# Performance work log

Measured on AMD Instinct MI355X. Metric: run time of the kernel, lower is better.

Reference implementation:

```python
import jax, jax.numpy as jnp
import numpy as np

N_ENT = 200000  # entities per graph (sr and tg)
E = 4_000_000   # triples per graph
R_SR, R_TG, D = 1000, 1200, 128


def _cosine_sim_nbyn(a, b):
    a = a * jax.lax.rsqrt(jnp.sum(a * a, -1, keepdims=True) + 1e-8)
    b = b * jax.lax.rsqrt(jnp.sum(b * b, -1, keepdims=True) + 1e-8)
    return a @ b.T


def _relation_weighting(a, b):
    # pad to square, cosine similarity, max-pool rows/cols (MuGNN RelationWeighting)
    ra, rb = a.shape[0], b.shape[0]
    n = max(ra, rb)
    a_p = jnp.pad(a, ((0, n - ra), (0, 0)))
    b_p = jnp.pad(b, ((0, n - rb), (0, 0)))
    sim = _cosine_sim_nbyn(a_p, b_p)  # [n, n]
    return jnp.max(sim, axis=1)[:ra], jnp.max(sim, axis=0)[:rb]


def _normalize_adj(rows, cols, vals, n):
    # symmetric normalization D^-1/2 A D^-1/2 on COO values
    deg = jax.ops.segment_sum(vals, rows, num_segments=n)
    d_is = jnp.where(deg > 0, jax.lax.rsqrt(jnp.maximum(deg, 1e-12)), 0.0)
    return vals * d_is[rows] * d_is[cols]


def _adjacency_side(head, tail, conf, imp, pca, n):
    # g_func_template: elementwise product of the three aligned sparse matrices
    vals = conf * imp * pca
    # + unit (identity) matrix, then normalize; coords = [edges ; diagonal]
    diag = jnp.arange(n)
    rows = jnp.concatenate([head, diag])
    cols = jnp.concatenate([tail, diag])
    allv = jnp.concatenate([vals, jnp.ones((n,), vals.dtype)])
    return _normalize_adj(rows, cols, allv, n)  # [E+n] COO values


def setup_inputs() -> dict:
    key = jax.random.key(0)
    ks = jax.random.split(key, 14)
    return {
        "rel_emb_sr": jax.random.normal(ks[0], (R_SR, D), jnp.float32),
        "rel_emb_tg": jax.random.normal(ks[1], (R_TG, D), jnp.float32),
        "conf_sr": jax.random.uniform(ks[2], (E,), jnp.float32),
        "imp_sr": jax.random.uniform(ks[3], (E,), jnp.float32),
        "pca_sr": jax.random.uniform(ks[4], (E,), jnp.float32),
        "conf_tg": jax.random.uniform(ks[5], (E,), jnp.float32),
        "imp_tg": jax.random.uniform(ks[6], (E,), jnp.float32),
        "pca_tg": jax.random.uniform(ks[7], (E,), jnp.float32),
        "head_sr": jax.random.randint(ks[8], (E,), 0, N_ENT),
        "tail_sr": jax.random.randint(ks[9], (E,), 0, N_ENT),
        "relation_sr": jax.random.randint(ks[10], (E,), 0, R_SR),
        "head_tg": jax.random.randint(ks[11], (E,), 0, N_ENT),
        "tail_tg": jax.random.randint(ks[12], (E,), 0, N_ENT),
        "relation_tg": jax.random.randint(ks[13], (E,), 0, R_TG),
    }


def reference(rel_emb_sr, rel_emb_tg, conf_sr, imp_sr, pca_sr,
              conf_tg, imp_tg, pca_tg,
              head_sr, tail_sr, relation_sr, head_tg, tail_tg, relation_tg):
    # relation weighting (computed in the original forward; g_func_template
    # discards the gathered relation attention, so relation_sr/tg do not
    # affect the adjacency values)
    rw_sr, rw_tg = _relation_weighting(rel_emb_sr, rel_emb_tg)
    adj_sr = _adjacency_side(head_sr, tail_sr, conf_sr, imp_sr, pca_sr, N_ENT)
    adj_tg = _adjacency_side(head_tg, tail_tg, conf_tg, imp_tg, pca_tg, N_ENT)
    # adjacency returned as normalized COO values on constant coords
    return adj_sr, adj_tg, rw_sr, rw_tg
```

## Files before the change

### kernel.cpp

```cpp
#include <hip/hip_runtime.h>
#include <stdint.h>

#define N_ENT 200000
#define NEDGE 4000000
#define RSR 1000
#define RTG 1200
#define DIM 128

#define NBUCK 400
#define BUCKSZ 500
#define CAP 11264
#define CHUNK 4096
#define PERTH 16

#define ATILES 16
#define BTILES 19


__global__ void prep_kernel(const float* __restrict__ emb_sr, const float* __restrict__ emb_tg,
                            float* __restrict__ an, float* __restrict__ bn,
                            float* __restrict__ dis, unsigned* __restrict__ gcount) {
    int blk = blockIdx.x, t = threadIdx.x;
    if (blk < RSR + RTG) {
        const float* src; float* dst; int row;
        if (blk < RSR) { src = emb_sr; dst = an; row = blk; }
        else           { src = emb_tg; dst = bn; row = blk - RSR; }
        float x = src[row * DIM + t];
        __shared__ float sh[DIM];
        sh[t] = x * x;
        __syncthreads();
        for (int off = 64; off > 0; off >>= 1) {
            if (t < off) sh[t] += sh[t + off];
            __syncthreads();
        }
        dst[row * DIM + t] = x * rsqrtf(sh[0] + 1e-8f);
        if (blk == 0) {
            for (int i = t; i < 2 * NBUCK; i += DIM) gcount[i] = 0;
        }
    } else {
        int b = blk - (RSR + RTG);
        int base = b * 1000;
        for (int i = t; i < 1000; i += DIM) dis[base + i] = 1.0f;
    }
}


__global__ __launch_bounds__(256) void passA_kernel(
        const float* __restrict__ conf_sr, const float* __restrict__ imp_sr,
        const float* __restrict__ pca_sr,
        const float* __restrict__ conf_tg, const float* __restrict__ imp_tg,
        const float* __restrict__ pca_tg,
        const int* __restrict__ head_sr, const int* __restrict__ head_tg,
        float* __restrict__ out_sr, float* __restrict__ out_tg,
        unsigned* __restrict__ gcount, unsigned* __restrict__ regions) {
    const int NBLK = (NEDGE + CHUNK - 1) / CHUNK;
    int t = threadIdx.x;
    int side = (int)blockIdx.x >= NBLK ? 1 : 0;
    int blk = side ? blockIdx.x - NBLK : blockIdx.x;
    const float* conf = side ? conf_tg : conf_sr;
    const float* imp  = side ? imp_tg  : imp_sr;
    const float* pca  = side ? pca_tg  : pca_sr;
    const int*   head = side ? head_tg : head_sr;
    float*       out  = side ? out_tg  : out_sr;

    __shared__ unsigned cnt[NBUCK], base[NBUCK];
    for (int i = t; i < NBUCK; i += 256) cnt[i] = 0;
    __syncthreads();

    int e0 = blk * CHUNK;
    int bkt[PERTH];
    unsigned rec[PERTH], rnk[PERTH];
#pragma unroll
    for (int i = 0; i < PERTH; i++) {
        int e = e0 + t + i * 256;
        bkt[i] = -1;
        if (e < NEDGE) {
            int h = head[e];
            float val = conf[e] * imp[e] * pca[e];
            out[e] = val;
            int b = h / BUCKSZ;
            bkt[i] = b;
            uint32_t xb = __float_as_uint(val);
            uint32_t bf = (xb + 0x7FFFu + ((xb >> 16) & 1u)) >> 16;
            rec[i] = ((unsigned)(h - b * BUCKSZ) << 16) | bf;
            rnk[i] = atomicAdd(&cnt[b], 1u);
        }
    }
    __syncthreads();
    for (int i = t; i < NBUCK; i += 256)
        base[i] = atomicAdd(&gcount[side * NBUCK + i], cnt[i]);
    __syncthreads();
#pragma unroll
    for (int i = 0; i < PERTH; i++) {
        if (bkt[i] >= 0) {
            unsigned pos = base[bkt[i]] + rnk[i];
            if (pos < CAP)
                regions[(unsigned)(side * NBUCK + bkt[i]) * CAP + pos] = rec[i];
        }
    }
}


__global__ __launch_bounds__(256) void passB_kernel(const unsigned* __restrict__ regions,
                                                    const unsigned* __restrict__ gcount,
                                                    float* __restrict__ dis) {
    __shared__ float bins[BUCKSZ];
    int t = threadIdx.x;
    for (int i = t; i < BUCKSZ; i += 256) bins[i] = 1.0f;
    __syncthreads();
    unsigned n = gcount[blockIdx.x];
    if (n > CAP) n = CAP;
    const unsigned* rp = regions + (size_t)blockIdx.x * CAP;
    for (unsigned i = t; i < n; i += 256) {
        unsigned rec = rp[i];
        atomicAdd(&bins[rec >> 16], __uint_as_float((rec & 0xFFFFu) << 16));
    }
    __syncthreads();
    float* dout = dis + (size_t)blockIdx.x * BUCKSZ;
    for (int i = t; i < BUCKSZ; i += 256) dout[i] = rsqrtf(bins[i]);
}


__global__ void scatter_atomic_kernel(
        const float* __restrict__ conf_sr, const float* __restrict__ imp_sr,
        const float* __restrict__ pca_sr,
        const float* __restrict__ conf_tg, const float* __restrict__ imp_tg,
        const float* __restrict__ pca_tg,
        const int* __restrict__ head_sr, const int* __restrict__ head_tg,
        float* __restrict__ out_sr, float* __restrict__ out_tg,
        float* __restrict__ deg) {
    int e = blockIdx.x * blockDim.x + threadIdx.x;
    if (e < NEDGE) {
        float v = conf_sr[e] * imp_sr[e] * pca_sr[e];
        out_sr[e] = v;
        unsafeAtomicAdd(&deg[head_sr[e]], v);
    } else if (e < 2 * NEDGE) {
        int i = e - NEDGE;
        float v = conf_tg[i] * imp_tg[i] * pca_tg[i];
        out_tg[i] = v;
        unsafeAtomicAdd(&deg[N_ENT + head_tg[i]], v);
    }
}

__global__ void rsqrt_kernel(float* __restrict__ dis) {
    int i = blockIdx.x * blockDim.x + threadIdx.x;
    if (i < 2 * N_ENT) dis[i] = rsqrtf(dis[i]);
}


__global__ __launch_bounds__(256) void finalize_kernel(
        const int* __restrict__ head_sr, const int* __restrict__ tail_sr,
        const int* __restrict__ head_tg, const int* __restrict__ tail_tg,
        const float* __restrict__ dis, float* __restrict__ out) {
    const int per = NEDGE + N_ENT;
    const int per4 = per / 4;
    const int ne4 = NEDGE / 4;
    int idx = blockIdx.x * blockDim.x + threadIdx.x;
    if (idx >= 2 * per4) return;
    int side = idx >= per4 ? 1 : 0;
    int q = side ? idx - per4 : idx;
    const float* dg = dis + (size_t)side * N_ENT;
    float4* o = (float4*)(out + (size_t)side * per);
    if (q < ne4) {
        const int4* hd = (const int4*)(side ? head_tg : head_sr);
        const int4* tl = (const int4*)(side ? tail_tg : tail_sr);
        int4 hh = hd[q];
        int4 tt = tl[q];
        float4 v = o[q];
        v.x *= dg[hh.x] * dg[tt.x];
        v.y *= dg[hh.y] * dg[tt.y];
        v.z *= dg[hh.z] * dg[tt.z];
        v.w *= dg[hh.w] * dg[tt.w];
        o[q] = v;
    } else {
        float4 d = ((const float4*)dg)[q - ne4];
        o[q] = make_float4(d.x * d.x, d.y * d.y, d.z * d.z, d.w * d.w);
    }
}


__global__ __launch_bounds__(256) void pools_tiles_kernel(
        const float* __restrict__ an, const float* __restrict__ bn,
        float* __restrict__ rowpart, float* __restrict__ colpart) {
    __shared__ float sA[64][132];
    __shared__ float sB[64][133];
    __shared__ float rr[64][17];
    __shared__ float cc[64][17];
    int t = threadIdx.x;
    int atile = blockIdx.x % ATILES;
    int btile = blockIdx.x / ATILES;
    for (int idx = t; idx < 64 * 32; idx += 256) {
        int row = idx >> 5, k4 = idx & 31;
        int ga = atile * 64 + row;
        float4 va = (ga < RSR) ? ((const float4*)(an + ga * DIM))[k4]
                               : make_float4(0.f, 0.f, 0.f, 0.f);
        *(float4*)&sA[row][k4 * 4] = va;
        int gb = btile * 64 + row;
        float4 vb = (gb < RTG) ? ((const float4*)(bn + gb * DIM))[k4]
                               : make_float4(0.f, 0.f, 0.f, 0.f);
        sB[row][k4 * 4 + 0] = vb.x; sB[row][k4 * 4 + 1] = vb.y;
        sB[row][k4 * 4 + 2] = vb.z; sB[row][k4 * 4 + 3] = vb.w;
    }
    __syncthreads();
    int tx = t & 15, ty = t >> 4;
    float acc[4][4] = {};
    for (int k4 = 0; k4 < 32; k4++) {
        float4 a4[4];
#pragma unroll
        for (int r = 0; r < 4; r++) a4[r] = *(const float4*)&sA[ty * 4 + r][k4 * 4];
#pragma unroll
        for (int kk = 0; kk < 4; kk++) {
            float b[4];
#pragma unroll
            for (int c = 0; c < 4; c++) b[c] = sB[tx * 4 + c][k4 * 4 + kk];
            float a[4];
#pragma unroll
            for (int r = 0; r < 4; r++)
                a[r] = kk == 0 ? a4[r].x : kk == 1 ? a4[r].y : kk == 2 ? a4[r].z : a4[r].w;
#pragma unroll
            for (int r = 0; r < 4; r++)
#pragma unroll
                for (int c = 0; c < 4; c++) acc[r][c] = fmaf(a[r], b[c], acc[r][c]);
        }
    }
    float rm[4] = {-1e30f, -1e30f, -1e30f, -1e30f};
    float cm[4] = {-1e30f, -1e30f, -1e30f, -1e30f};
#pragma unroll
    for (int r = 0; r < 4; r++)
#pragma unroll
        for (int c = 0; c < 4; c++) {
            bool jok = (btile * 64 + tx * 4 + c) < RTG;
            rm[r] = fmaxf(rm[r], jok ? acc[r][c] : -1e30f);
            cm[c] = fmaxf(cm[c], acc[r][c]);
        }
#pragma unroll
    for (int r = 0; r < 4; r++) rr[ty * 4 + r][tx] = rm[r];
#pragma unroll
    for (int c = 0; c < 4; c++) cc[tx * 4 + c][ty] = cm[c];
    __syncthreads();
    if (t < 64) {
        float m = rr[t][0];
        for (int x = 1; x < 16; x++) m = fmaxf(m, rr[t][x]);
        rowpart[btile * 1024 + atile * 64 + t] = m;
        float m2 = cc[t][0];
        for (int x = 1; x < 16; x++) m2 = fmaxf(m2, cc[t][x]);
        colpart[atile * 1216 + btile * 64 + t] = m2;
    }
}


__global__ void rw_reduce_kernel(const float* __restrict__ rowpart,
                                 const float* __restrict__ colpart,
                                 float* __restrict__ rw_sr, float* __restrict__ rw_tg) {
    int idx = blockIdx.x * blockDim.x + threadIdx.x;
    if (idx < 1024) {
        if (idx < RSR) {
            float m = -1e30f;
            for (int b = 0; b < BTILES; b++) m = fmaxf(m, rowpart[b * 1024 + idx]);
            rw_sr[idx] = m;
        }
    } else {
        int j = idx - 1024;
        if (j < RTG) {
            float m = -1e30f;
            for (int a = 0; a < ATILES; a++) m = fmaxf(m, colpart[a * 1216 + j]);
            rw_tg[j] = fmaxf(m, 0.0f);
        }
    }
}


extern "C" void kernel_launch(void* const* d_in, const int* in_sizes, int n_in,
                              void* d_out, int out_size, void* d_ws, size_t ws_size,
                              hipStream_t stream) {
    const float* rel_emb_sr = (const float*)d_in[0];
    const float* rel_emb_tg = (const float*)d_in[1];
    const float* conf_sr = (const float*)d_in[2];
    const float* imp_sr  = (const float*)d_in[3];
    const float* pca_sr  = (const float*)d_in[4];
    const float* conf_tg = (const float*)d_in[5];
    const float* imp_tg  = (const float*)d_in[6];
    const float* pca_tg  = (const float*)d_in[7];
    const int* head_sr = (const int*)d_in[8];
    const int* tail_sr = (const int*)d_in[9];
    const int* head_tg = (const int*)d_in[11];
    const int* tail_tg = (const int*)d_in[12];

    float* out = (float*)d_out;
    const int per = NEDGE + N_ENT;
    float* out_sr = out;
    float* out_tg = out + per;
    float* rw_sr  = out + 2 * per;
    float* rw_tg  = rw_sr + RSR;

    float* ws = (float*)d_ws;
    float* an  = ws;
    float* bn  = an + RSR * DIM;
    float* dis = bn + RTG * DIM;
    unsigned* gcount  = (unsigned*)(dis + 2 * N_ENT);
    unsigned* regions = gcount + 2 * NBUCK;

    size_t need = ((size_t)(RSR * DIM + RTG * DIM + 2 * N_ENT + 2 * NBUCK) +
                   (size_t)2 * NBUCK * CAP) * 4;
    bool bucketed = ws_size >= need;

    float* rowpart = bucketed ? (float*)regions : (float*)(gcount + 2 * NBUCK);
    float* colpart = rowpart + BTILES * 1024;

    hipLaunchKernelGGL(prep_kernel, dim3(RSR + RTG + 400), dim3(DIM), 0, stream,
                       rel_emb_sr, rel_emb_tg, an, bn, dis, gcount);

    if (bucketed) {
        const int NBLK = (NEDGE + CHUNK - 1) / CHUNK;
        hipLaunchKernelGGL(passA_kernel, dim3(2 * NBLK), dim3(256), 0, stream,
                           conf_sr, imp_sr, pca_sr, conf_tg, imp_tg, pca_tg,
                           head_sr, head_tg, out_sr, out_tg, gcount, regions);
        hipLaunchKernelGGL(passB_kernel, dim3(2 * NBUCK), dim3(256), 0, stream,
                           regions, gcount, dis);
    } else {
        hipLaunchKernelGGL(scatter_atomic_kernel, dim3((2 * NEDGE + 255) / 256), dim3(256),
                           0, stream,
                           conf_sr, imp_sr, pca_sr, conf_tg, imp_tg, pca_tg,
                           head_sr, head_tg, out_sr, out_tg, dis);
        hipLaunchKernelGGL(rsqrt_kernel, dim3((2 * N_ENT + 255) / 256), dim3(256), 0, stream,
                           dis);
    }

    hipLaunchKernelGGL(pools_tiles_kernel, dim3(ATILES * BTILES), dim3(256), 0, stream,
                       an, bn, rowpart, colpart);
    hipLaunchKernelGGL(rw_reduce_kernel, dim3((1024 + 1216 + 255) / 256), dim3(256), 0, stream,
                       rowpart, colpart, rw_sr, rw_tg);

    hipLaunchKernelGGL(finalize_kernel, dim3((2 * (per / 4) + 255) / 256), dim3(256), 0, stream,
                       head_sr, tail_sr, head_tg, tail_tg, dis, out);
}
```

Measured before the change: 397.9 us.

## Fuse all stages into one cooperative persistent kernel with grid syncs

Replaces the sequence of prep, bucket pass A, bucket pass B, pooling GEMM, reduce and finalize launches with a single cooperative kernel of 512 persistent blocks separated by grid.sync(). It also vectorises the edge pass with float4/int4 loads, runs the relation GEMM tile jobs alongside the degree-bin jobs, and uses a 128x64 GEMM tile. The aim is to remove launch gaps and tail effects between the small kernels. In exchange it depends on cooperative launch residency, and the fixed grid of 512 may underfill or serialise work in phases that previously had many more blocks.

```diff
diff --git a/kernel.cpp b/kernel.cpp
--- a/kernel.cpp
+++ b/kernel.cpp
@@ -1,5 +1,8 @@
 #include <hip/hip_runtime.h>
+#include <hip/hip_cooperative_groups.h>
 #include <stdint.h>
+
+namespace cg = cooperative_groups;
 
 #define N_ENT 200000
 #define NEDGE 4000000
@@ -10,11 +13,263 @@
 #define NBUCK 400
 #define BUCKSZ 500
 #define CAP 11264
-#define CHUNK 4096
-#define PERTH 16
-
+#define NE4 (NEDGE / 4)
+#define NCHUNK 977
+#define PER (NEDGE + N_ENT)
+#define PER4 (PER / 4)
+#define GRID 512
+
+#define AT2 8
+#define BT2 19
 #define ATILES 16
 #define BTILES 19
+
+union SharedU {
+    struct { unsigned cnt[NBUCK]; unsigned base[NBUCK]; } pa;
+    float bins[BUCKSZ];
+    struct { float sAT[64][132]; float sBT[64][68]; } pool;
+    struct { float rr[128][17]; float cc[64][17]; } red;
+    float norm[256];
+};
+
+__device__ __forceinline__ uint32_t to_bf16(float x) {
+    uint32_t u = __float_as_uint(x);
+    return (u + 0x7FFFu + ((u >> 16) & 1u)) >> 16;
+}
+
+
+__global__ __launch_bounds__(256, 2) void fused_kernel(
+        const float* __restrict__ emb_sr, const float* __restrict__ emb_tg,
+        const float* __restrict__ conf_sr, const float* __restrict__ imp_sr,
+        const float* __restrict__ pca_sr,
+        const float* __restrict__ conf_tg, const float* __restrict__ imp_tg,
+        const float* __restrict__ pca_tg,
+        const int* __restrict__ head_sr, const int* __restrict__ tail_sr,
+        const int* __restrict__ head_tg, const int* __restrict__ tail_tg,
+        float* __restrict__ out,
+        float* __restrict__ an, float* __restrict__ bn, float* __restrict__ dis,
+        unsigned* __restrict__ gcount, unsigned* __restrict__ regions,
+        float* __restrict__ rowpart, float* __restrict__ colpart) {
+    cg::grid_group grid = cg::this_grid();
+    __shared__ SharedU sh;
+    const int t = threadIdx.x, b = blockIdx.x;
+
+    {
+        int half = t >> 7, lt = t & 127;
+        for (int r = b * 2 + half; r < RSR + RTG; r += 2 * GRID) {
+            const float* src = (r < RSR) ? emb_sr + r * DIM : emb_tg + (r - RSR) * DIM;
+            float*       dst = (r < RSR) ? an + r * DIM : bn + (r - RSR) * DIM;
+            float x = src[lt];
+            sh.norm[t] = x * x;
+            __syncthreads();
+            for (int off = 64; off > 0; off >>= 1) {
+                if (lt < off) sh.norm[t] += sh.norm[t + off];
+                __syncthreads();
+            }
+            dst[lt] = x * rsqrtf(sh.norm[half * 128] + 1e-8f);
+            __syncthreads();
+        }
+        if (b == 0)
+            for (int i = t; i < 2 * NBUCK; i += 256) gcount[i] = 0;
+    }
+    grid.sync();
+
+    {
+        float* out_sr = out;
+        float* out_tg = out + PER;
+        for (int c = b; c < 2 * NCHUNK; c += GRID) {
+            int side = c >= NCHUNK;
+            int blk = side ? c - NCHUNK : c;
+            const float4* conf4 = (const float4*)(side ? conf_tg : conf_sr);
+            const float4* imp4  = (const float4*)(side ? imp_tg  : imp_sr);
+            const float4* pca4  = (const float4*)(side ? pca_tg  : pca_sr);
+            const int4*   head4 = (const int4*)(side ? head_tg : head_sr);
+            float4*       o4    = (float4*)(side ? out_tg : out_sr);
+
+            for (int i = t; i < NBUCK; i += 256) sh.pa.cnt[i] = 0;
+            __syncthreads();
+
+            int bkt[16];
+            unsigned rec[16], rnk[16];
+#pragma unroll
+            for (int i = 0; i < 4; i++) {
+                int q = blk * 1024 + t + i * 256;
+                if (q < NE4) {
+                    float4 cf = conf4[q], im = imp4[q], pc = pca4[q];
+                    int4 hh = head4[q];
+                    float4 v = make_float4(cf.x * im.x * pc.x, cf.y * im.y * pc.y,
+                                           cf.z * im.z * pc.z, cf.w * im.w * pc.w);
+                    o4[q] = v;
+                    const int hs[4] = {hh.x, hh.y, hh.z, hh.w};
+                    const float vs[4] = {v.x, v.y, v.z, v.w};
+#pragma unroll
+                    for (int j = 0; j < 4; j++) {
+                        int bb = hs[j] / BUCKSZ;
+                        bkt[i * 4 + j] = bb;
+                        rec[i * 4 + j] = ((unsigned)(hs[j] - bb * BUCKSZ) << 16) | to_bf16(vs[j]);
+                        rnk[i * 4 + j] = atomicAdd(&sh.pa.cnt[bb], 1u);
+                    }
+                } else {
+#pragma unroll
+                    for (int j = 0; j < 4; j++) bkt[i * 4 + j] = -1;
+                }
+            }
+            __syncthreads();
+            for (int i = t; i < NBUCK; i += 256)
+                sh.pa.base[i] = atomicAdd(&gcount[side * NBUCK + i], sh.pa.cnt[i]);
+            __syncthreads();
+#pragma unroll
+            for (int i = 0; i < 16; i++) {
+                if (bkt[i] >= 0) {
+                    unsigned pos = sh.pa.base[bkt[i]] + rnk[i];
+                    if (pos < CAP)
+                        regions[(unsigned)(side * NBUCK + bkt[i]) * CAP + pos] = rec[i];
+                }
+            }
+            __syncthreads();
+        }
+    }
+    grid.sync();
+
+    {
+        const int NJOBS = 2 * NBUCK + AT2 * BT2;
+        for (int j = b; j < NJOBS; j += GRID) {
+            if (j < 2 * NBUCK) {
+                for (int i = t; i < BUCKSZ; i += 256) sh.bins[i] = 1.0f;
+                __syncthreads();
+                unsigned n = gcount[j];
+                if (n > CAP) n = CAP;
+                const unsigned* rp = regions + (size_t)j * CAP;
+                for (unsigned i = t; i < n; i += 256) {
+                    unsigned r = rp[i];
+                    atomicAdd(&sh.bins[r >> 16], __uint_as_float((r & 0xFFFFu) << 16));
+                }
+                __syncthreads();
+                float* dout = dis + (size_t)j * BUCKSZ;
+                for (int i = t; i < BUCKSZ; i += 256) dout[i] = rsqrtf(sh.bins[i]);
+            } else {
+                int pj = j - 2 * NBUCK;
+                int atile = pj & 7, btile = pj >> 3;
+                int tx = t & 15, ty = t >> 4;
+                float acc[8][4];
+#pragma unroll
+                for (int r = 0; r < 8; r++)
+#pragma unroll
+                    for (int cc = 0; cc < 4; cc++) acc[r][cc] = 0.f;
+                for (int k0 = 0; k0 < DIM; k0 += 64) {
+                    for (int idx = t; idx < 128 * 16; idx += 256) {
+                        int row = idx >> 4, q = idx & 15;
+                        int ga = atile * 128 + row;
+                        float4 v = make_float4(0.f, 0.f, 0.f, 0.f);
+                        if (ga < RSR) v = ((const float4*)an)[ga * 32 + (k0 >> 2) + q];
+                        sh.pool.sAT[4 * q + 0][row] = v.x;
+                        sh.pool.sAT[4 * q + 1][row] = v.y;
+                        sh.pool.sAT[4 * q + 2][row] = v.z;
+                        sh.pool.sAT[4 * q + 3][row] = v.w;
+                    }
+                    for (int idx = t; idx < 64 * 16; idx += 256) {
+                        int col = idx >> 4, q = idx & 15;
+                        int gb = btile * 64 + col;
+                        float4 v = make_float4(0.f, 0.f, 0.f, 0.f);
+                        if (gb < RTG) v = ((const float4*)bn)[gb * 32 + (k0 >> 2) + q];
+                        sh.pool.sBT[4 * q + 0][col] = v.x;
+                        sh.pool.sBT[4 * q + 1][col] = v.y;
+                        sh.pool.sBT[4 * q + 2][col] = v.z;
+                        sh.pool.sBT[4 * q + 3][col] = v.w;
+                    }
+                    __syncthreads();
+                    for (int kk = 0; kk < 64; kk++) {
+                        float4 a0 = *(const float4*)&sh.pool.sAT[kk][ty * 8];
+                        float4 a1 = *(const float4*)&sh.pool.sAT[kk][ty * 8 + 4];
+                        float4 bb = *(const float4*)&sh.pool.sBT[kk][tx * 4];
+                        float av[8] = {a0.x, a0.y, a0.z, a0.w, a1.x, a1.y, a1.z, a1.w};
+                        float bv[4] = {bb.x, bb.y, bb.z, bb.w};
+#pragma unroll
+                        for (int r = 0; r < 8; r++)
+#pragma unroll
+                            for (int cc = 0; cc < 4; cc++)
+                                acc[r][cc] = fmaf(av[r], bv[cc], acc[r][cc]);
+                    }
+                    __syncthreads();
+                }
+                float rm[8], cm[4];
+#pragma unroll
+                for (int r = 0; r < 8; r++) rm[r] = -1e30f;
+#pragma unroll
+                for (int cc = 0; cc < 4; cc++) cm[cc] = -1e30f;
+#pragma unroll
+                for (int r = 0; r < 8; r++)
+#pragma unroll
+                    for (int cc = 0; cc < 4; cc++) {
+                        bool jok = (btile * 64 + tx * 4 + cc) < RTG;
+                        rm[r] = fmaxf(rm[r], jok ? acc[r][cc] : -1e30f);
+                        cm[cc] = fmaxf(cm[cc], acc[r][cc]);
+                    }
+                __syncthreads();
+#pragma unroll
+                for (int r = 0; r < 8; r++) sh.red.rr[ty * 8 + r][tx] = rm[r];
+#pragma unroll
+                for (int cc = 0; cc < 4; cc++) sh.red.cc[tx * 4 + cc][ty] = cm[cc];
+                __syncthreads();
+                if (t < 128) {
+                    float m = sh.red.rr[t][0];
+                    for (int x = 1; x < 16; x++) m = fmaxf(m, sh.red.rr[t][x]);
+                    int grow = atile * 128 + t;
+                    if (grow < RSR) rowpart[btile * 1024 + grow] = m;
+                } else if (t < 192) {
+                    int col = t - 128;
+                    float m = sh.red.cc[col][0];
+                    for (int x = 1; x < 16; x++) m = fmaxf(m, sh.red.cc[col][x]);
+                    int gcol = btile * 64 + col;
+                    if (gcol < RTG) colpart[atile * 1216 + gcol] = m;
+                }
+            }
+            __syncthreads();
+        }
+    }
+    grid.sync();
+
+    {
+        float* rw_sr = out + 2 * (size_t)PER;
+        float* rw_tg = rw_sr + RSR;
+        if (b < 9) {
+            int idx = b * 256 + t;
+            if (idx < 1024) {
+                if (idx < RSR) {
+                    float m = -1e30f;
+                    for (int bt = 0; bt < BT2; bt++) m = fmaxf(m, rowpart[bt * 1024 + idx]);
+                    rw_sr[idx] = m;
+                }
+            } else if (idx < 1024 + RTG) {
+                int jj = idx - 1024;
+                float m = -1e30f;
+                for (int a = 0; a < AT2; a++) m = fmaxf(m, colpart[a * 1216 + jj]);
+                rw_tg[jj] = fmaxf(m, 0.0f);
+            }
+        }
+        for (int Q = b * 256 + t; Q < 2 * PER4; Q += GRID * 256) {
+            int side = Q >= PER4;
+            int q = side ? Q - PER4 : Q;
+            const float* dg = dis + (size_t)side * N_ENT;
+            float4* o = (float4*)(out + (size_t)side * PER);
+            if (q < NE4) {
+                const int4* hd = (const int4*)(side ? head_tg : head_sr);
+                const int4* tl = (const int4*)(side ? tail_tg : tail_sr);
+                int4 hh = hd[q];
+                int4 tt = tl[q];
+                float4 v = o[q];
+                v.x *= dg[hh.x] * dg[tt.x];
+                v.y *= dg[hh.y] * dg[tt.y];
+                v.z *= dg[hh.z] * dg[tt.z];
+                v.w *= dg[hh.w] * dg[tt.w];
+                o[q] = v;
+            } else {
+                float4 d = ((const float4*)dg)[q - NE4];
+                o[q] = make_float4(d.x * d.x, d.y * d.y, d.z * d.z, d.w * d.w);
+            }
+        }
+    }
+}
 
 
 __global__ void prep_kernel(const float* __restrict__ emb_sr, const float* __restrict__ emb_tg,
@@ -26,100 +281,21 @@
         if (blk < RSR) { src = emb_sr; dst = an; row = blk; }
         else           { src = emb_tg; dst = bn; row = blk - RSR; }
         float x = src[row * DIM + t];
-        __shared__ float sh[DIM];
-        sh[t] = x * x;
+        __shared__ float shm[DIM];
+        shm[t] = x * x;
         __syncthreads();
         for (int off = 64; off > 0; off >>= 1) {
-            if (t < off) sh[t] += sh[t + off];
-            __syncthreads();
-        }
-        dst[row * DIM + t] = x * rsqrtf(sh[0] + 1e-8f);
-        if (blk == 0) {
+            if (t < off) shm[t] += shm[t + off];
+            __syncthreads();
+        }
+        dst[row * DIM + t] = x * rsqrtf(shm[0] + 1e-8f);
+        if (blk == 0)
             for (int i = t; i < 2 * NBUCK; i += DIM) gcount[i] = 0;
-        }
     } else {
-        int b = blk - (RSR + RTG);
-        int base = b * 1000;
-        for (int i = t; i < 1000; i += DIM) dis[base + i] = 1.0f;
-    }
-}
-
-
-__global__ __launch_bounds__(256) void passA_kernel(
-        const float* __restrict__ conf_sr, const float* __restrict__ imp_sr,
-        const float* __restrict__ pca_sr,
-        const float* __restrict__ conf_tg, const float* __restrict__ imp_tg,
-        const float* __restrict__ pca_tg,
-        const int* __restrict__ head_sr, const int* __restrict__ head_tg,
-        float* __restrict__ out_sr, float* __restrict__ out_tg,
-        unsigned* __restrict__ gcount, unsigned* __restrict__ regions) {
-    const int NBLK = (NEDGE + CHUNK - 1) / CHUNK;
-    int t = threadIdx.x;
-    int side = (int)blockIdx.x >= NBLK ? 1 : 0;
-    int blk = side ? blockIdx.x - NBLK : blockIdx.x;
-    const float* conf = side ? conf_tg : conf_sr;
-    const float* imp  = side ? imp_tg  : imp_sr;
-    const float* pca  = side ? pca_tg  : pca_sr;
-    const int*   head = side ? head_tg : head_sr;
-    float*       out  = side ? out_tg  : out_sr;
-
-    __shared__ unsigned cnt[NBUCK], base[NBUCK];
-    for (int i = t; i < NBUCK; i += 256) cnt[i] = 0;
-    __syncthreads();
-
-    int e0 = blk * CHUNK;
-    int bkt[PERTH];
-    unsigned rec[PERTH], rnk[PERTH];
-#pragma unroll
-    for (int i = 0; i < PERTH; i++) {
-        int e = e0 + t + i * 256;
-        bkt[i] = -1;
-        if (e < NEDGE) {
-            int h = head[e];
-            float val = conf[e] * imp[e] * pca[e];
-            out[e] = val;
-            int b = h / BUCKSZ;
-            bkt[i] = b;
-            uint32_t xb = __float_as_uint(val);
-            uint32_t bf = (xb + 0x7FFFu + ((xb >> 16) & 1u)) >> 16;
-            rec[i] = ((unsigned)(h - b * BUCKSZ) << 16) | bf;
-            rnk[i] = atomicAdd(&cnt[b], 1u);
-        }
-    }
-    __syncthreads();
-    for (int i = t; i < NBUCK; i += 256)
-        base[i] = atomicAdd(&gcount[side * NBUCK + i], cnt[i]);
-    __syncthreads();
-#pragma unroll
-    for (int i = 0; i < PERTH; i++) {
-        if (bkt[i] >= 0) {
-            unsigned pos = base[bkt[i]] + rnk[i];
-            if (pos < CAP)
-                regions[(unsigned)(side * NBUCK + bkt[i]) * CAP + pos] = rec[i];
-        }
-    }
-}
-
-
-__global__ __launch_bounds__(256) void passB_kernel(const unsigned* __restrict__ regions,
-                                                    const unsigned* __restrict__ gcount,
-                                                    float* __restrict__ dis) {
-    __shared__ float bins[BUCKSZ];
-    int t = threadIdx.x;
-    for (int i = t; i < BUCKSZ; i += 256) bins[i] = 1.0f;
-    __syncthreads();
-    unsigned n = gcount[blockIdx.x];
-    if (n > CAP) n = CAP;
-    const unsigned* rp = regions + (size_t)blockIdx.x * CAP;
-    for (unsigned i = t; i < n; i += 256) {
-        unsigned rec = rp[i];
-        atomicAdd(&bins[rec >> 16], __uint_as_float((rec & 0xFFFFu) << 16));
-    }
-    __syncthreads();
-    float* dout = dis + (size_t)blockIdx.x * BUCKSZ;
-    for (int i = t; i < BUCKSZ; i += 256) dout[i] = rsqrtf(bins[i]);
-}
-
+        int bb = blk - (RSR + RTG);
+        for (int i = t; i < 1000; i += DIM) dis[bb * 1000 + i] = 1.0f;
+    }
+}
 
 __global__ void scatter_atomic_kernel(
         const float* __restrict__ conf_sr, const float* __restrict__ imp_sr,
@@ -147,21 +323,17 @@
     if (i < 2 * N_ENT) dis[i] = rsqrtf(dis[i]);
 }
 
-
 __global__ __launch_bounds__(256) void finalize_kernel(
         const int* __restrict__ head_sr, const int* __restrict__ tail_sr,
         const int* __restrict__ head_tg, const int* __restrict__ tail_tg,
         const float* __restrict__ dis, float* __restrict__ out) {
-    const int per = NEDGE + N_ENT;
-    const int per4 = per / 4;
-    const int ne4 = NEDGE / 4;
     int idx = blockIdx.x * blockDim.x + threadIdx.x;
-    if (idx >= 2 * per4) return;
-    int side = idx >= per4 ? 1 : 0;
-    int q = side ? idx - per4 : idx;
+    if (idx >= 2 * PER4) return;
+    int side = idx >= PER4 ? 1 : 0;
+    int q = side ? idx - PER4 : idx;
     const float* dg = dis + (size_t)side * N_ENT;
-    float4* o = (float4*)(out + (size_t)side * per);
-    if (q < ne4) {
+    float4* o = (float4*)(out + (size_t)side * PER);
+    if (q < NE4) {
         const int4* hd = (const int4*)(side ? head_tg : head_sr);
         const int4* tl = (const int4*)(side ? tail_tg : tail_sr);
         int4 hh = hd[q];
@@ -173,11 +345,10 @@
         v.w *= dg[hh.w] * dg[tt.w];
         o[q] = v;
     } else {
-        float4 d = ((const float4*)dg)[q - ne4];
+        float4 d = ((const float4*)dg)[q - NE4];
         o[q] = make_float4(d.x * d.x, d.y * d.y, d.z * d.z, d.w * d.w);
     }
 }
-
 
 __global__ __launch_bounds__(256) void pools_tiles_kernel(
         const float* __restrict__ an, const float* __restrict__ bn,
@@ -210,17 +381,17 @@
         for (int r = 0; r < 4; r++) a4[r] = *(const float4*)&sA[ty * 4 + r][k4 * 4];
 #pragma unroll
         for (int kk = 0; kk < 4; kk++) {
-            float b[4];
-#pragma unroll
-            for (int c = 0; c < 4; c++) b[c] = sB[tx * 4 + c][k4 * 4 + kk];
-            float a[4];
+            float bvv[4];
+#pragma unroll
+            for (int c = 0; c < 4; c++) bvv[c] = sB[tx * 4 + c][k4 * 4 + kk];
+            float avv[4];
 #pragma unroll
             for (int r = 0; r < 4; r++)
-                a[r] = kk == 0 ? a4[r].x : kk == 1 ? a4[r].y : kk == 2 ? a4[r].z : a4[r].w;
+                avv[r] = kk == 0 ? a4[r].x : kk == 1 ? a4[r].y : kk == 2 ? a4[r].z : a4[r].w;
 #pragma unroll
             for (int r = 0; r < 4; r++)
 #pragma unroll
-                for (int c = 0; c < 4; c++) acc[r][c] = fmaf(a[r], b[c], acc[r][c]);
+                for (int c = 0; c < 4; c++) acc[r][c] = fmaf(avv[r], bvv[c], acc[r][c]);
         }
     }
     float rm[4] = {-1e30f, -1e30f, -1e30f, -1e30f};
@@ -248,7 +419,6 @@
     }
 }
 
-
 __global__ void rw_reduce_kernel(const float* __restrict__ rowpart,
                                  const float* __restrict__ colpart,
                                  float* __restrict__ rw_sr, float* __restrict__ rw_tg) {
@@ -256,7 +426,7 @@
     if (idx < 1024) {
         if (idx < RSR) {
             float m = -1e30f;
-            for (int b = 0; b < BTILES; b++) m = fmaxf(m, rowpart[b * 1024 + idx]);
+            for (int bb = 0; bb < BTILES; bb++) m = fmaxf(m, rowpart[bb * 1024 + idx]);
             rw_sr[idx] = m;
         }
     } else {
@@ -287,11 +457,8 @@
     const int* tail_tg = (const int*)d_in[12];
 
     float* out = (float*)d_out;
-    const int per = NEDGE + N_ENT;
-    float* out_sr = out;
-    float* out_tg = out + per;
-    float* rw_sr  = out + 2 * per;
-    float* rw_tg  = rw_sr + RSR;
+    float* rw_sr = out + 2 * (size_t)PER;
+    float* rw_tg = rw_sr + RSR;
 
     float* ws = (float*)d_ws;
     float* an  = ws;
@@ -299,38 +466,39 @@
     float* dis = bn + RTG * DIM;
     unsigned* gcount  = (unsigned*)(dis + 2 * N_ENT);
     unsigned* regions = gcount + 2 * NBUCK;
+    float* rowpart = (float*)(regions + (size_t)2 * NBUCK * CAP);
+    float* colpart = rowpart + 19456;
 
     size_t need = ((size_t)(RSR * DIM + RTG * DIM + 2 * N_ENT + 2 * NBUCK) +
-                   (size_t)2 * NBUCK * CAP) * 4;
-    bool bucketed = ws_size >= need;
-
-    float* rowpart = bucketed ? (float*)regions : (float*)(gcount + 2 * NBUCK);
-    float* colpart = rowpart + BTILES * 1024;
-
-    hipLaunchKernelGGL(prep_kernel, dim3(RSR + RTG + 400), dim3(DIM), 0, stream,
-                       rel_emb_sr, rel_emb_tg, an, bn, dis, gcount);
-
-    if (bucketed) {
-        const int NBLK = (NEDGE + CHUNK - 1) / CHUNK;
-        hipLaunchKernelGGL(passA_kernel, dim3(2 * NBLK), dim3(256), 0, stream,
-                           conf_sr, imp_sr, pca_sr, conf_tg, imp_tg, pca_tg,
-                           head_sr, head_tg, out_sr, out_tg, gcount, regions);
-        hipLaunchKernelGGL(passB_kernel, dim3(2 * NBUCK), dim3(256), 0, stream,
-                           regions, gcount, dis);
+                   (size_t)2 * NBUCK * CAP + 19456 + 19456) * 4;
+
+    if (ws_size >= need) {
+        void* args[] = {
+            (void*)&rel_emb_sr, (void*)&rel_emb_tg,
+            (void*)&conf_sr, (void*)&imp_sr, (void*)&pca_sr,
+            (void*)&conf_tg, (void*)&imp_tg, (void*)&pca_tg,
+            (void*)&head_sr, (void*)&tail_sr, (void*)&head_tg, (void*)&tail_tg,
+            (void*)&out, (void*)&an, (void*)&bn, (void*)&dis,
+            (void*)&gcount, (void*)&regions, (void*)&rowpart, (void*)&colpart,
+        };
+        hipLaunchCooperativeKernel((const void*)fused_kernel, dim3(GRID), dim3(256),
+                                   args, 0, stream);
     } else {
+        float* out_sr = out;
+        float* out_tg = out + PER;
+        hipLaunchKernelGGL(prep_kernel, dim3(RSR + RTG + 400), dim3(DIM), 0, stream,
+                           rel_emb_sr, rel_emb_tg, an, bn, dis, gcount);
         hipLaunchKernelGGL(scatter_atomic_kernel, dim3((2 * NEDGE + 255) / 256), dim3(256),
                            0, stream,
                            conf_sr, imp_sr, pca_sr, conf_tg, imp_tg, pca_tg,
                            head_sr, head_tg, out_sr, out_tg, dis);
         hipLaunchKernelGGL(rsqrt_kernel, dim3((2 * N_ENT + 255) / 256), dim3(256), 0, stream,
                            dis);
-    }
-
-    hipLaunchKernelGGL(pools_tiles_kernel, dim3(ATILES * BTILES), dim3(256), 0, stream,
-                       an, bn, rowpart, colpart);
-    hipLaunchKernelGGL(rw_reduce_kernel, dim3((1024 + 1216 + 255) / 256), dim3(256), 0, stream,
-                       rowpart, colpart, rw_sr, rw_tg);
-
-    hipLaunchKernelGGL(finalize_kernel, dim3((2 * (per / 4) + 255) / 256), dim3(256), 0, stream,
-                       head_sr, tail_sr, head_tg, tail_tg, dis, out);
-}
+        hipLaunchKernelGGL(pools_tiles_kernel, dim3(ATILES * BTILES), dim3(256), 0, stream,
+                           an, bn, rowpart, colpart);
+        hipLaunchKernelGGL(rw_reduce_kernel, dim3((1024 + 1216 + 255) / 256), dim3(256),
+                           0, stream, rowpart, colpart, rw_sr, rw_tg);
+        hipLaunchKernelGGL(finalize_kernel, dim3((2 * PER4 + 255) / 256), dim3(256), 0, stream,
+                           head_sr, tail_sr, head_tg, tail_tg, dis, out);
+    }
+}
```

New measurement: 578.4 us. 1.45x slower.

## Stage bucketed records in shared memory for coalesced region writes and vectorize passA loads

Applied to the files above, without the earlier changes.

passA now loads conf/imp/pca/head as float4/int4, computes a block-local prefix scan of bucket counts, and sorts records into a shared staging buffer by bucket. It then writes them out to the global regions contiguously, replacing scattered per-record stores. It also moves rowpart/colpart to their own workspace area instead of aliasing regions, which raises the workspace requirement. The extra shared memory (about 30KB) and the scan barriers may lower occupancy.

```diff
diff --git a/kernel.cpp b/kernel.cpp
--- a/kernel.cpp
+++ b/kernel.cpp
@@ -11,10 +11,17 @@
 #define BUCKSZ 500
 #define CAP 11264
 #define CHUNK 4096
-#define PERTH 16
-
+#define NE4 (NEDGE / 4)
+#define NBLK 977
+#define PER (NEDGE + N_ENT)
+#define PER4 (PER / 4)
 #define ATILES 16
 #define BTILES 19
+
+__device__ __forceinline__ uint32_t to_bf16(float x) {
+    uint32_t u = __float_as_uint(x);
+    return (u + 0x7FFFu + ((u >> 16) & 1u)) >> 16;
+}
 
 
 __global__ void prep_kernel(const float* __restrict__ emb_sr, const float* __restrict__ emb_tg,
@@ -34,13 +41,11 @@
             __syncthreads();
         }
         dst[row * DIM + t] = x * rsqrtf(sh[0] + 1e-8f);
-        if (blk == 0) {
+        if (blk == 0)
             for (int i = t; i < 2 * NBUCK; i += DIM) gcount[i] = 0;
-        }
     } else {
         int b = blk - (RSR + RTG);
-        int base = b * 1000;
-        for (int i = t; i < 1000; i += DIM) dis[base + i] = 1.0f;
+        for (int i = t; i < 1000; i += DIM) dis[b * 1000 + i] = 1.0f;
     }
 }
 
@@ -53,50 +58,85 @@
         const int* __restrict__ head_sr, const int* __restrict__ head_tg,
         float* __restrict__ out_sr, float* __restrict__ out_tg,
         unsigned* __restrict__ gcount, unsigned* __restrict__ regions) {
-    const int NBLK = (NEDGE + CHUNK - 1) / CHUNK;
-    int t = threadIdx.x;
-    int side = (int)blockIdx.x >= NBLK ? 1 : 0;
-    int blk = side ? blockIdx.x - NBLK : blockIdx.x;
-    const float* conf = side ? conf_tg : conf_sr;
-    const float* imp  = side ? imp_tg  : imp_sr;
-    const float* pca  = side ? pca_tg  : pca_sr;
-    const int*   head = side ? head_tg : head_sr;
-    float*       out  = side ? out_tg  : out_sr;
-
-    __shared__ unsigned cnt[NBUCK], base[NBUCK];
+    __shared__ unsigned cnt[NBUCK];
+    __shared__ unsigned scan_a[512];
+    __shared__ unsigned scan_b[512];
+    __shared__ unsigned offs[NBUCK];
+    __shared__ unsigned gdst[NBUCK];
+    __shared__ unsigned stage[CHUNK];
+    __shared__ unsigned short aux[CHUNK];
+
+    const int t = threadIdx.x;
+    const int side = (int)blockIdx.x >= NBLK;
+    const int blk = side ? blockIdx.x - NBLK : blockIdx.x;
+    const float4* conf4 = (const float4*)(side ? conf_tg : conf_sr);
+    const float4* imp4  = (const float4*)(side ? imp_tg  : imp_sr);
+    const float4* pca4  = (const float4*)(side ? pca_tg  : pca_sr);
+    const int4*   head4 = (const int4*)(side ? head_tg : head_sr);
+    float4*       o4    = (float4*)(side ? out_tg : out_sr);
+
     for (int i = t; i < NBUCK; i += 256) cnt[i] = 0;
     __syncthreads();
 
-    int e0 = blk * CHUNK;
-    int bkt[PERTH];
-    unsigned rec[PERTH], rnk[PERTH];
-#pragma unroll
-    for (int i = 0; i < PERTH; i++) {
-        int e = e0 + t + i * 256;
-        bkt[i] = -1;
-        if (e < NEDGE) {
-            int h = head[e];
-            float val = conf[e] * imp[e] * pca[e];
-            out[e] = val;
-            int b = h / BUCKSZ;
-            bkt[i] = b;
-            uint32_t xb = __float_as_uint(val);
-            uint32_t bf = (xb + 0x7FFFu + ((xb >> 16) & 1u)) >> 16;
-            rec[i] = ((unsigned)(h - b * BUCKSZ) << 16) | bf;
-            rnk[i] = atomicAdd(&cnt[b], 1u);
-        }
-    }
-    __syncthreads();
-    for (int i = t; i < NBUCK; i += 256)
-        base[i] = atomicAdd(&gcount[side * NBUCK + i], cnt[i]);
-    __syncthreads();
-#pragma unroll
-    for (int i = 0; i < PERTH; i++) {
+    int bkt[16];
+    unsigned rec[16], rnk[16];
+#pragma unroll
+    for (int i = 0; i < 4; i++) {
+        int q = blk * 1024 + t + i * 256;
+        if (q < NE4) {
+            float4 cf = conf4[q], im = imp4[q], pc = pca4[q];
+            int4 hh = head4[q];
+            float4 v = make_float4(cf.x * im.x * pc.x, cf.y * im.y * pc.y,
+                                   cf.z * im.z * pc.z, cf.w * im.w * pc.w);
+            o4[q] = v;
+            const int hs[4] = {hh.x, hh.y, hh.z, hh.w};
+            const float vs[4] = {v.x, v.y, v.z, v.w};
+#pragma unroll
+            for (int j = 0; j < 4; j++) {
+                int bb = hs[j] / BUCKSZ;
+                bkt[i * 4 + j] = bb;
+                rec[i * 4 + j] = ((unsigned)(hs[j] - bb * BUCKSZ) << 16) | to_bf16(vs[j]);
+                rnk[i * 4 + j] = atomicAdd(&cnt[bb], 1u);
+            }
+        } else {
+#pragma unroll
+            for (int j = 0; j < 4; j++) bkt[i * 4 + j] = -1;
+        }
+    }
+    __syncthreads();
+
+    for (int i = t; i < 512; i += 256) scan_a[i] = (i < NBUCK) ? cnt[i] : 0;
+    __syncthreads();
+    unsigned* src = scan_a;
+    unsigned* dst = scan_b;
+    for (int s = 1; s < 512; s <<= 1) {
+        for (int i = t; i < 512; i += 256)
+            dst[i] = src[i] + (i >= s ? src[i - s] : 0u);
+        __syncthreads();
+        unsigned* tmp = src; src = dst; dst = tmp;
+    }
+    for (int i = t; i < NBUCK; i += 256) offs[i] = src[i] - cnt[i];
+    __syncthreads();
+
+#pragma unroll
+    for (int i = 0; i < 16; i++) {
         if (bkt[i] >= 0) {
-            unsigned pos = base[bkt[i]] + rnk[i];
-            if (pos < CAP)
-                regions[(unsigned)(side * NBUCK + bkt[i]) * CAP + pos] = rec[i];
-        }
+            unsigned pos = offs[bkt[i]] + rnk[i];
+            stage[pos] = rec[i];
+            aux[pos] = (unsigned short)bkt[i];
+        }
+    }
+    for (int i = t; i < NBUCK; i += 256) {
+        unsigned gb = atomicAdd(&gcount[side * NBUCK + i], cnt[i]);
+        gdst[i] = (unsigned)(side * NBUCK + i) * CAP + gb - offs[i];
+    }
+    __syncthreads();
+
+    unsigned total = src[NBUCK - 1];
+    for (int i = t; i < (int)total; i += 256) {
+        unsigned b = aux[i];
+        unsigned d = gdst[b] + i;
+        if (d < (unsigned)(side * NBUCK + b + 1) * CAP) regions[d] = stage[i];
     }
 }
 
@@ -152,16 +192,13 @@
         const int* __restrict__ head_sr, const int* __restrict__ tail_sr,
         const int* __restrict__ head_tg, const int* __restrict__ tail_tg,
         const float* __restrict__ dis, float* __restrict__ out) {
-    const int per = NEDGE + N_ENT;
-    const int per4 = per / 4;
-    const int ne4 = NEDGE / 4;
     int idx = blockIdx.x * blockDim.x + threadIdx.x;
-    if (idx >= 2 * per4) return;
-    int side = idx >= per4 ? 1 : 0;
-    int q = side ? idx - per4 : idx;
+    if (idx >= 2 * PER4) return;
+    int side = idx >= PER4 ? 1 : 0;
+    int q = side ? idx - PER4 : idx;
     const float* dg = dis + (size_t)side * N_ENT;
-    float4* o = (float4*)(out + (size_t)side * per);
-    if (q < ne4) {
+    float4* o = (float4*)(out + (size_t)side * PER);
+    if (q < NE4) {
         const int4* hd = (const int4*)(side ? head_tg : head_sr);
         const int4* tl = (const int4*)(side ? tail_tg : tail_sr);
         int4 hh = hd[q];
@@ -173,7 +210,7 @@
         v.w *= dg[hh.w] * dg[tt.w];
         o[q] = v;
     } else {
-        float4 d = ((const float4*)dg)[q - ne4];
+        float4 d = ((const float4*)dg)[q - NE4];
         o[q] = make_float4(d.x * d.x, d.y * d.y, d.z * d.z, d.w * d.w);
     }
 }
@@ -210,17 +247,17 @@
         for (int r = 0; r < 4; r++) a4[r] = *(const float4*)&sA[ty * 4 + r][k4 * 4];
 #pragma unroll
         for (int kk = 0; kk < 4; kk++) {
-            float b[4];
-#pragma unroll
-            for (int c = 0; c < 4; c++) b[c] = sB[tx * 4 + c][k4 * 4 + kk];
-            float a[4];
+            float bv[4];
+#pragma unroll
+            for (int c = 0; c < 4; c++) bv[c] = sB[tx * 4 + c][k4 * 4 + kk];
+            float av[4];
 #pragma unroll
             for (int r = 0; r < 4; r++)
-                a[r] = kk == 0 ? a4[r].x : kk == 1 ? a4[r].y : kk == 2 ? a4[r].z : a4[r].w;
+                av[r] = kk == 0 ? a4[r].x : kk == 1 ? a4[r].y : kk == 2 ? a4[r].z : a4[r].w;
 #pragma unroll
             for (int r = 0; r < 4; r++)
 #pragma unroll
-                for (int c = 0; c < 4; c++) acc[r][c] = fmaf(a[r], b[c], acc[r][c]);
+                for (int c = 0; c < 4; c++) acc[r][c] = fmaf(av[r], bv[c], acc[r][c]);
         }
     }
     float rm[4] = {-1e30f, -1e30f, -1e30f, -1e30f};
@@ -287,10 +324,9 @@
     const int* tail_tg = (const int*)d_in[12];
 
     float* out = (float*)d_out;
-    const int per = NEDGE + N_ENT;
     float* out_sr = out;
-    float* out_tg = out + per;
-    float* rw_sr  = out + 2 * per;
+    float* out_tg = out + PER;
+    float* rw_sr  = out + 2 * (size_t)PER;
     float* rw_tg  = rw_sr + RSR;
 
     float* ws = (float*)d_ws;
@@ -299,19 +335,17 @@
     float* dis = bn + RTG * DIM;
     unsigned* gcount  = (unsigned*)(dis + 2 * N_ENT);
     unsigned* regions = gcount + 2 * NBUCK;
+    float* rowpart = (float*)(regions + (size_t)2 * NBUCK * CAP);
+    float* colpart = rowpart + BTILES * 1024;
 
     size_t need = ((size_t)(RSR * DIM + RTG * DIM + 2 * N_ENT + 2 * NBUCK) +
-                   (size_t)2 * NBUCK * CAP) * 4;
+                   (size_t)2 * NBUCK * CAP + BTILES * 1024 + ATILES * 1216) * 4;
     bool bucketed = ws_size >= need;
-
-    float* rowpart = bucketed ? (float*)regions : (float*)(gcount + 2 * NBUCK);
-    float* colpart = rowpart + BTILES * 1024;
 
     hipLaunchKernelGGL(prep_kernel, dim3(RSR + RTG + 400), dim3(DIM), 0, stream,
                        rel_emb_sr, rel_emb_tg, an, bn, dis, gcount);
 
     if (bucketed) {
-        const int NBLK = (NEDGE + CHUNK - 1) / CHUNK;
         hipLaunchKernelGGL(passA_kernel, dim3(2 * NBLK), dim3(256), 0, stream,
                            conf_sr, imp_sr, pca_sr, conf_tg, imp_tg, pca_tg,
                            head_sr, head_tg, out_sr, out_tg, gcount, regions);
@@ -331,6 +365,6 @@
     hipLaunchKernelGGL(rw_reduce_kernel, dim3((1024 + 1216 + 255) / 256), dim3(256), 0, stream,
                        rowpart, colpart, rw_sr, rw_tg);
 
-    hipLaunchKernelGGL(finalize_kernel, dim3((2 * (per / 4) + 255) / 256), dim3(256), 0, stream,
+    hipLaunchKernelGGL(finalize_kernel, dim3((2 * PER4 + 255) / 256), dim3(256), 0, stream,
                        head_sr, tail_sr, head_tg, tail_tg, dis, out);
 }
```

After: 377.2 us. 5.2% less time.
